# Kernel tuning notes

Hardware: AMD Instinct MI355X
Metric: run time of the kernel (lower is better)

The kernel has to match this reference:

```python
import jax, jax.numpy as jnp
import numpy as np

K = 3          # deformable conv kernel size
PAD = 1        # padding
BN_EPS = 1e-5


def _upsample2(x):
    # nn.Upsample(scale_factor=2) default mode='nearest' on [B,C,D,H,W]
    x = jnp.repeat(x, 2, axis=2)
    x = jnp.repeat(x, 2, axis=3)
    x = jnp.repeat(x, 2, axis=4)
    return x


def _conv3d(x, w, b):
    out = jax.lax.conv_general_dilated(
        x, w, window_strides=(1, 1, 1), padding=[(PAD, PAD)] * 3,
        dimension_numbers=('NCDHW', 'OIDHW', 'NCDHW'))
    return out + b[None, :, None, None, None]


def _trilinear_sample(x, coords):
    # x: [B,C,D,H,W]; coords: [B,Kt,3,D,H,W] absolute (possibly OOB) positions.
    # Zero padding outside the volume (standard deformable-conv convention).
    B, C, D, H, W = x.shape
    pd, ph, pw = coords[:, :, 0], coords[:, :, 1], coords[:, :, 2]  # [B,Kt,D,H,W]
    d0 = jnp.floor(pd); h0 = jnp.floor(ph); w0 = jnp.floor(pw)
    fd = pd - d0; fh = ph - h0; fw = pw - w0
    x_flat = x.reshape(B, C, D * H * W)

    def gather(di, hi, wi):
        valid = ((di >= 0) & (di < D) & (hi >= 0) & (hi < H) & (wi >= 0) & (wi < W))
        dc = jnp.clip(di, 0, D - 1).astype(jnp.int32)
        hc = jnp.clip(hi, 0, H - 1).astype(jnp.int32)
        wc = jnp.clip(wi, 0, W - 1).astype(jnp.int32)
        flat = (dc * H + hc) * W + wc                       # [B,Kt,D,H,W]
        vals = jax.vmap(lambda xf, idx: jnp.take(xf, idx.reshape(-1), axis=1))(x_flat, flat)
        vals = vals.reshape(B, C, *flat.shape[1:])          # [B,C,Kt,D,H,W]
        return vals * valid[:, None].astype(x.dtype)

    out = jnp.zeros((B, C) + pd.shape[1:], x.dtype)
    for dd in (0, 1):
        for hh in (0, 1):
            for ww in (0, 1):
                wgt = ((fd if dd else 1.0 - fd)
                       * (fh if hh else 1.0 - fh)
                       * (fw if ww else 1.0 - fw))           # [B,Kt,D,H,W]
                out = out + gather(d0 + dd, h0 + hh, w0 + ww) * wgt[:, None]
    return out  # [B,C,Kt,D,H,W]


def _deform_conv3d(x, w_off, b_off, w, b):
    B, C, D, H, W = x.shape
    Kt = K ** 3
    # offsets: Conv3d(C, 3*K^3, k=3, pad=1) -> [B, Kt, 3(dz,dy,dx), D,H,W]
    off = _conv3d(x, w_off, b_off).reshape(B, Kt, 3, D, H, W)
    # kernel tap displacements relative to output voxel: [Kt,3]
    taps = jnp.stack(jnp.meshgrid(jnp.arange(K), jnp.arange(K), jnp.arange(K),
                                  indexing='ij'), -1).reshape(-1, 3).astype(x.dtype) - PAD
    grid = jnp.stack(jnp.meshgrid(jnp.arange(D, dtype=x.dtype),
                                  jnp.arange(H, dtype=x.dtype),
                                  jnp.arange(W, dtype=x.dtype),
                                  indexing='ij'), 0)          # [3,D,H,W]
    coords = grid[None, None] + taps[None, :, :, None, None, None] + off  # [B,Kt,3,D,H,W]
    sampled = _trilinear_sample(x, coords)                    # [B,C,Kt,D,H,W]
    out = jnp.einsum('bckdhw,ock->bodhw', sampled, w.reshape(w.shape[0], C, Kt))
    return out + b[None, :, None, None, None]


def setup_inputs() -> dict:
    key = jax.random.key(0)
    ks = jax.random.split(key, 4)
    ch_in, ch_out = 64, 32
    x = jax.random.normal(ks[0], (1, ch_in, 16, 16, 16), jnp.float32)
    w_off = jax.random.normal(ks[1], (3 * K ** 3, ch_in, K, K, K), jnp.float32) * 0.01
    b_off = jnp.zeros((3 * K ** 3,), jnp.float32)
    w = jax.random.normal(ks[2], (ch_out, ch_in, K, K, K), jnp.float32) * 0.05
    b = jnp.zeros((ch_out,), jnp.float32)
    gamma = jnp.ones((ch_out,), jnp.float32)
    beta = jnp.zeros((ch_out,), jnp.float32)
    return {"x": x, "w_off": w_off, "b_off": b_off, "w": w, "b": b,
            "gamma": gamma, "beta": beta}


def reference(x, w_off, b_off, w, b, gamma, beta):
    x = _upsample2(x)                                  # [B,C,2D,2H,2W]
    out = _deform_conv3d(x, w_off, b_off, w, b)        # [B,ch_out,2D,2H,2W]
    # BatchNorm3d (training-mode batch stats) + ReLU
    mean = out.mean(axis=(0, 2, 3, 4), keepdims=True)
    var = out.var(axis=(0, 2, 3, 4), keepdims=True)
    out = (out - mean) * jax.lax.rsqrt(var + BN_EPS)
    out = out * gamma[None, :, None, None, None] + beta[None, :, None, None, None]
    return jax.nn.relu(out)
```

## Files before the change

kernel.cpp:

```cpp
#include <hip/hip_runtime.h>
#include <math.h>

#define NVOX  32768
#define CIN   64
#define COUT  32
#define KT    27
#define CIT   1728
#define PSP   5832

#define WS_XT   0
#define WS_WA   186624
#define WS_WO   214272
#define WS_STAT 297216
#define WS_P    297280

typedef __attribute__((ext_vector_type(8))) _Float16 half8;
typedef __attribute__((ext_vector_type(2))) _Float16 half2v;
typedef __attribute__((ext_vector_type(4))) float floatx4;

static __device__ __forceinline__ unsigned dup16(float w) {
    unsigned short b = __builtin_bit_cast(unsigned short, (_Float16)w);
    return (unsigned)b * 0x10001u;
}
static __device__ __forceinline__ half2v u2h2(unsigned u) {
    return __builtin_bit_cast(half2v, u);
}
static __device__ __forceinline__ half8 pk8(half2v a, half2v b, half2v c, half2v d) {
    union { half8 v; half2v p[4]; } u;
    u.p[0] = a; u.p[1] = b; u.p[2] = c; u.p[3] = d;
    return u.v;
}

__global__ __launch_bounds__(256) void prep_all_kernel(
        const float* __restrict__ x, const float* __restrict__ w_off,
        const float* __restrict__ wmat, float* __restrict__ ws) {
    int b = blockIdx.x, t = threadIdx.x;
    if (b < 92) {
        __shared__ _Float16 tile[64][65];
        _Float16* xth = (_Float16*)(ws + WS_XT);
        int tq = t >> 6, lane = t & 63;
        int base = b * 64;
        int cell = base + lane;
        int qw = cell % 18, qh = (cell / 18) % 18, qd = cell / 324;
        bool interior = (cell < PSP) && qd >= 1 && qd <= 16 && qh >= 1 && qh <= 16
                        && qw >= 1 && qw <= 16;
        int xbase = interior ? (((qd - 1) * 16 + (qh - 1)) * 16 + (qw - 1)) : 0;
#pragma unroll
        for (int i = 0; i < 16; i++) {
            int c = tq * 16 + i;
            float v = interior ? x[c * 4096 + xbase] : 0.f;
            tile[lane][c] = (_Float16)v;
        }
        __syncthreads();
#pragma unroll
        for (int i = 0; i < 16; i++) {
            int s = tq * 16 + i;
            int cell2 = base + s;
            if (cell2 < PSP) xth[cell2 * 64 + lane] = tile[s][lane];
        }
    } else if (b < 119) {
        _Float16* wa = (_Float16*)(ws + WS_WA);
        int idx = (b - 92) * 256 + t;
        int kb = idx >> 5, o = idx & 31;
        half8 r;
#pragma unroll
        for (int j = 0; j < 8; j++) {
            int kk = kb * 8 + j;
            int tap = kk >> 6, ci = kk & 63;
            r[j] = (_Float16)wmat[o * CIT + ci * 27 + tap];
        }
        *(half8*)(wa + idx * 8) = r;
    } else if (b < 200) {
        _Float16* wo = (_Float16*)(ws + WS_WO);
        int idx = (b - 119) * 256 + t;
        int kb = idx / 96, m = idx % 96;
        half8 r;
#pragma unroll
        for (int j = 0; j < 8; j++) {
            int kk = kb * 8 + j;
            int tap = kk >> 6, ci = kk & 63;
            float v = (m < 81) ? w_off[(m * 64 + ci) * 27 + tap] : 0.f;
            r[j] = (_Float16)v;
        }
        *(half8*)(wo + idx * 8) = r;
    } else {
        if (t < 64) ws[WS_STAT + t] = 0.f;
    }
}

__global__ __launch_bounds__(256, 4) void offset_kernel(
        const float* __restrict__ b_off, float* ws) {
    __shared__ __align__(16) _Float16 abuf[2 * 6144];
    int tid = threadIdx.x, wave = tid >> 6, lane = tid & 63;
    int nsub = wave & 1, kh = wave >> 1;
    int col = lane & 15, quad = lane >> 4;
    int pbase = blockIdx.x * 32;
    int d = blockIdx.x >> 5, h = blockIdx.x & 31;
    int vox = nsub * 16 + col;
    const char* xtb = (const char*)(ws + WS_XT);
    const int4* wsrc = (const int4*)(ws + WS_WO);
    _Float16* Pw = (_Float16*)(ws + WS_P);
    int4* ab4 = (int4*)abuf;

    int4 ra0 = wsrc[tid], ra1 = wsrc[256 + tid], ra2 = wsrc[512 + tid];
    ab4[tid] = ra0; ab4[256 + tid] = ra1; ab4[512 + tid] = ra2;
    ra0 = wsrc[768 + tid]; ra1 = wsrc[768 + 256 + tid]; ra2 = wsrc[768 + 512 + tid];
    __syncthreads();

    floatx4 acc[6];
#pragma unroll
    for (int mt = 0; mt < 6; mt++) acc[mt] = (floatx4){0.f, 0.f, 0.f, 0.f};

    int fb = (kh * 4 + quad) * 768 + col * 8;

#pragma unroll 1
    for (int tap = 0; tap < 27; tap++) {
        if (tap < 26) {
            int4* dst = ab4 + ((tap + 1) & 1) * 768;
            dst[tid] = ra0; dst[256 + tid] = ra1; dst[512 + tid] = ra2;
        }
        if (tap < 25) {
            const int4* s = wsrc + (tap + 2) * 768;
            ra0 = s[tid]; ra1 = s[256 + tid]; ra2 = s[512 + tid];
        }
        int kd = tap / 9, r9 = tap - kd * 9, kh2 = r9 / 3, kw2 = r9 - kh2 * 3;
        int rd = ((d + kd - 1) >> 1) + 1;
        int rh = ((h + kh2 - 1) >> 1) + 1;
        int rw = ((vox + kw2 - 1) >> 1) + 1;
        int cell = (rd * 18 + rh) * 18 + rw;
        int4 bx = *(const int4*)(xtb + cell * 128 + kh * 64 + quad * 16);
        half8 bfrag = __builtin_bit_cast(half8, bx);
        const _Float16* abh = abuf + (tap & 1) * 6144;
#pragma unroll
        for (int mt = 0; mt < 6; mt++) {
            half8 af = *(const half8*)(abh + fb + mt * 128);
            acc[mt] = __builtin_amdgcn_mfma_f32_16x16x32_f16(af, bfrag, acc[mt], 0, 0, 0);
        }
        __syncthreads();
    }

    float* red = (float*)abuf;
    if (kh == 1) {
#pragma unroll
        for (int mt = 0; mt < 6; mt++)
#pragma unroll
            for (int r = 0; r < 4; r++)
                red[(nsub * 96 + mt * 16 + quad * 4 + r) * 17 + col] = acc[mt][r];
    }
    __syncthreads();
    if (kh == 0) {
#pragma unroll
        for (int mt = 0; mt < 6; mt++)
#pragma unroll
            for (int r = 0; r < 4; r++) {
                int m = mt * 16 + quad * 4 + r;
                if (m < 81) {
                    float v = acc[mt][r] + red[(nsub * 96 + m) * 17 + col] + b_off[m];
                    Pw[m * NVOX + pbase + nsub * 16 + col] = (_Float16)v;
                }
            }
    }
}

#define ACCP(xl, xh, Wx) do { \
    s00 += (Wx) * u2h2((unsigned)(xl).x); s01 += (Wx) * u2h2((unsigned)(xl).y); \
    s02 += (Wx) * u2h2((unsigned)(xl).z); s03 += (Wx) * u2h2((unsigned)(xl).w); \
    s10 += (Wx) * u2h2((unsigned)(xh).x); s11 += (Wx) * u2h2((unsigned)(xh).y); \
    s12 += (Wx) * u2h2((unsigned)(xh).z); s13 += (Wx) * u2h2((unsigned)(xh).w); \
} while (0)

#define DO2(ap, wp) do { \
    int a0_ = (ap) & 0x7fff, a1_ = (int)((((unsigned)(ap)) >> 16) & 0x7fffu); \
    unsigned wl_ = ((unsigned)(wp) & 0xffffu) * 0x10001u; \
    unsigned wh_ = (((unsigned)(wp)) >> 16) * 0x10001u; \
    int4 x0l_ = *(const int4*)(region + (a0_ ^ subLo)); \
    int4 x0h_ = *(const int4*)(region + (a0_ ^ subHi)); \
    int4 x1l_ = *(const int4*)(region + (a1_ ^ subLo)); \
    int4 x1h_ = *(const int4*)(region + (a1_ ^ subHi)); \
    ACCP(x0l_, x0h_, u2h2(wl_)); ACCP(x1l_, x1h_, u2h2(wh_)); \
} while (0)

#define GSLOW(Ax, wf) do { \
    half2v Wq_ = u2h2(dup16(wf)); \
    int4 xl_ = *(const int4*)(xtb + (Ax) + subLo); \
    int4 xh_ = *(const int4*)(xtb + (Ax) + subLo + 64); \
    t00 += Wq_ * u2h2((unsigned)xl_.x); t01 += Wq_ * u2h2((unsigned)xl_.y); \
    t02 += Wq_ * u2h2((unsigned)xl_.z); t03 += Wq_ * u2h2((unsigned)xl_.w); \
    t10 += Wq_ * u2h2((unsigned)xh_.x); t11 += Wq_ * u2h2((unsigned)xh_.y); \
    t12 += Wq_ * u2h2((unsigned)xh_.z); t13 += Wq_ * u2h2((unsigned)xh_.w); \
} while (0)

__global__ __launch_bounds__(256, 4) void deform_kernel(
        const float* __restrict__ bias, float* ws, float* __restrict__ out) {
    __shared__ __align__(16) char region[25600];
    __shared__ __align__(16) int2 scratch[4][16][4];
    __shared__ float pbuf[2][2][16][17];
    __shared__ float rsum[COUT], rsq[COUT];

    int tid = threadIdx.x, wave = tid >> 6, lane = tid & 63;
    int col = lane & 15, quad = lane >> 4;
    int bid = blockIdx.x;
    int d0 = (bid >> 6) << 1, h0 = ((bid >> 2) & 15) << 1, w0 = (bid & 3) << 3;

    const char* xtb = (const char*)(ws + WS_XT);
    const half8* wa8 = (const half8*)(ws + WS_WA);
    const _Float16* P = (const _Float16*)(ws + WS_P);
    float* gstat = ws + WS_STAT;

    if (tid < COUT) { rsum[tid] = 0.f; rsq[tid] = 0.f; }

    int pdlo = (d0 >> 1) - 1, phlo = (h0 >> 1) - 1, pwlo = (w0 >> 1) - 1;

#pragma unroll 1
    for (int it = 0; it < 7; it++) {
        int i = it * 256 + tid;
        if (i < 1600) {
            int r = i >> 3, c16 = i & 7;
            int rd = r / 40, rem = r - rd * 40, rh = rem >> 3, rw = rem & 7;
            int pd = min(max(pdlo + rd, 0), 17);
            int ph = min(max(phlo + rh, 0), 17);
            int pw = min(max(pwlo + rw, 0), 17);
            int cell = (pd * 18 + ph) * 18 + pw;
            int4 vsrc = *(const int4*)(xtb + cell * 128 + c16 * 16);
            *(int4*)(region + r * 128 + ((c16 * 16) ^ ((r & 7) << 4))) = vsrc;
        }
    }
    __syncthreads();

    int vh = wave & 1, kt = wave >> 1;
    int v = vh * 16 + col;
    int dv = v >> 4, hv = (v >> 3) & 1, wv = v & 7;
    int dcoord = d0 + dv, hcoord = h0 + hv, wcoord = w0 + wv;
    int gvox = dcoord * 1024 + hcoord * 32 + wcoord;
    int tbeg = kt ? 14 : 0, tend = kt ? 27 : 14;
    int subLo = quad * 16, subHi = subLo + 64;
    int bd = quad >> 1, bh = quad & 1;

    floatx4 acc0 = {0.f, 0.f, 0.f, 0.f}, acc1 = {0.f, 0.f, 0.f, 0.f};

    float od = (float)P[(3 * tbeg + 0) * NVOX + gvox];
    float oh = (float)P[(3 * tbeg + 1) * NVOX + gvox];
    float ow = (float)P[(3 * tbeg + 2) * NVOX + gvox];

#pragma unroll 1
    for (int tap = tbeg; tap < tend; tap++) {
        int kd = tap / 9, r9 = tap - kd * 9, kh2 = r9 / 3, kw2 = r9 - kh2 * 3;
        float pdc = (float)(dcoord + kd - 1) + od;
        float phc = (float)(hcoord + kh2 - 1) + oh;
        float pwc = (float)(wcoord + kw2 - 1) + ow;
        float fd0 = floorf(pdc), fh0 = floorf(phc), fw0 = floorf(pwc);
        float fd = pdc - fd0, fh = phc - fh0, fw = pwc - fw0;
        int id = (int)fd0, ih = (int)fh0, iw = (int)fw0;

        int cd0 = ((min(max(id,     -2), 33)) >> 1) + 1;
        int cd1 = ((min(max(id + 1, -2), 33)) >> 1) + 1;
        int ch0 = ((min(max(ih,     -2), 33)) >> 1) + 1;
        int ch1 = ((min(max(ih + 1, -2), 33)) >> 1) + 1;
        int cw0 = ((min(max(iw,     -2), 33)) >> 1) + 1;
        int cw1 = ((min(max(iw + 1, -2), 33)) >> 1) + 1;
        int sd0 = cd0 - pdlo, sd1 = cd1 - pdlo;
        int sh0 = ch0 - phlo, sh1 = ch1 - phlo;
        int sw0 = cw0 - pwlo, sw1 = cw1 - pwlo;
        bool oob = ((unsigned)sd0 > 4u) | ((unsigned)sd1 > 4u)
                 | ((unsigned)sh0 > 4u) | ((unsigned)sh1 > 4u)
                 | ((unsigned)sw0 > 7u) | ((unsigned)sw1 > 7u);

        int sdq = bd ? sd1 : sd0, shq = bh ? sh1 : sh0;
        int rb = (sdq * 5 + shq) * 8;
        int r0 = rb + sw0, r1 = rb + sw1;
        int a0 = oob ? 0x8000 : ((r0 << 7) | ((r0 & 7) << 4));
        int a1 = oob ? 0x8000 : ((r1 << 7) | ((r1 & 7) << 4));
        float gdw = 1.f - fd, ghw = 1.f - fh, gww = 1.f - fw;
        float wd = bd ? fd : gdw, wh = bh ? fh : ghw;
        float wdh = wd * wh;
        unsigned wb0 = (unsigned)__builtin_bit_cast(unsigned short, (_Float16)(wdh * gww));
        unsigned wb1 = (unsigned)__builtin_bit_cast(unsigned short, (_Float16)(wdh * fw));
        scratch[wave][col][quad] = make_int2(a0 | (a1 << 16), (int)(wb0 | (wb1 << 16)));

        if (tap + 1 < tend) {
            od = (float)P[(3 * tap + 3) * NVOX + gvox];
            oh = (float)P[(3 * tap + 4) * NVOX + gvox];
            ow = (float)P[(3 * tap + 5) * NVOX + gvox];
        }

        int kb = tap * 8 + quad;
        half8 a00 = wa8[kb * 32 + col];
        half8 a01 = wa8[kb * 32 + 16 + col];
        half8 a10 = wa8[(kb + 4) * 32 + col];
        half8 a11 = wa8[(kb + 4) * 32 + 16 + col];

        const int4* sc = (const int4*)&scratch[wave][col][0];
        int4 p0 = sc[0], p1 = sc[1];

        half2v s00 = {0, 0}, s01 = {0, 0}, s02 = {0, 0}, s03 = {0, 0};
        half2v s10 = {0, 0}, s11 = {0, 0}, s12 = {0, 0}, s13 = {0, 0};
        DO2(p0.x, p0.y); DO2(p0.z, p0.w);
        DO2(p1.x, p1.y); DO2(p1.z, p1.w);

        if (__any((p0.x & 0x8000) != 0)) {
            bool flg = (p0.x & 0x8000) != 0;
            int Rd0 = ((min(max(id,     -2), 33) >> 1) + 1) * (324 * 128);
            int Rd1 = ((min(max(id + 1, -2), 33) >> 1) + 1) * (324 * 128);
            int Rh0 = ((min(max(ih,     -2), 33) >> 1) + 1) * (18 * 128);
            int Rh1 = ((min(max(ih + 1, -2), 33) >> 1) + 1) * (18 * 128);
            int Rw0 = ((min(max(iw,     -2), 33) >> 1) + 1) * 128;
            int Rw1 = ((min(max(iw + 1, -2), 33) >> 1) + 1) * 128;
            half2v t00 = {0,0}, t01 = {0,0}, t02 = {0,0}, t03 = {0,0};
            half2v t10 = {0,0}, t11 = {0,0}, t12 = {0,0}, t13 = {0,0};
            GSLOW(Rd0 + Rh0 + Rw0, gdw * ghw * gww);
            GSLOW(Rd0 + Rh0 + Rw1, gdw * ghw * fw);
            GSLOW(Rd0 + Rh1 + Rw0, gdw * fh  * gww);
            GSLOW(Rd0 + Rh1 + Rw1, gdw * fh  * fw);
            GSLOW(Rd1 + Rh0 + Rw0, fd  * ghw * gww);
            GSLOW(Rd1 + Rh0 + Rw1, fd  * ghw * fw);
            GSLOW(Rd1 + Rh1 + Rw0, fd  * fh  * gww);
            GSLOW(Rd1 + Rh1 + Rw1, fd  * fh  * fw);
            s00 = flg ? t00 : s00; s01 = flg ? t01 : s01;
            s02 = flg ? t02 : s02; s03 = flg ? t03 : s03;
            s10 = flg ? t10 : s10; s11 = flg ? t11 : s11;
            s12 = flg ? t12 : s12; s13 = flg ? t13 : s13;
        }

        half8 bf0 = pk8(s00, s01, s02, s03);
        half8 bf1 = pk8(s10, s11, s12, s13);

        acc0 = __builtin_amdgcn_mfma_f32_16x16x32_f16(a00, bf0, acc0, 0, 0, 0);
        acc1 = __builtin_amdgcn_mfma_f32_16x16x32_f16(a01, bf0, acc1, 0, 0, 0);
        acc0 = __builtin_amdgcn_mfma_f32_16x16x32_f16(a10, bf1, acc0, 0, 0, 0);
        acc1 = __builtin_amdgcn_mfma_f32_16x16x32_f16(a11, bf1, acc1, 0, 0, 0);
    }

    __syncthreads();
    if (kt == 1) {
#pragma unroll
        for (int r = 0; r < 4; r++) {
            pbuf[vh][0][quad * 4 + r][col] = acc0[r];
            pbuf[vh][1][quad * 4 + r][col] = acc1[r];
        }
    }
    __syncthreads();
    if (kt == 0) {
#pragma unroll
        for (int r = 0; r < 4; r++) {
            int i = quad * 4 + r;
            int o0 = i;
            float v0 = acc0[r] + pbuf[vh][0][i][col] + bias[o0];
            out[o0 * NVOX + gvox] = v0;
            atomicAdd(&rsum[o0], v0);
            atomicAdd(&rsq[o0], v0 * v0);
            int o1 = 16 + i;
            float v1 = acc1[r] + pbuf[vh][1][i][col] + bias[o1];
            out[o1 * NVOX + gvox] = v1;
            atomicAdd(&rsum[o1], v1);
            atomicAdd(&rsq[o1], v1 * v1);
        }
    }
    __syncthreads();
    if (tid < COUT) {
        atomicAdd(&gstat[tid], rsum[tid]);
        atomicAdd(&gstat[COUT + tid], rsq[tid]);
    }
}

__global__ void bn_kernel(const float* __restrict__ ws,
                          const float* __restrict__ gamma,
                          const float* __restrict__ beta,
                          float* out) {
    int i = blockIdx.x * 256 + threadIdx.x;
    int o = i >> 15;
    const float* gstat = ws + WS_STAT;
    const float inv = 1.f / 32768.f;
    float mean = gstat[o] * inv;
    float var  = gstat[COUT + o] * inv - mean * mean;
    float sc   = rsqrtf(var + 1e-5f) * gamma[o];
    float v = (out[i] - mean) * sc + beta[o];
    out[i] = fmaxf(v, 0.f);
}

extern "C" void kernel_launch(void* const* d_in, const int* in_sizes, int n_in,
                              void* d_out, int out_size, void* d_ws, size_t ws_size,
                              hipStream_t stream) {
    const float* x     = (const float*)d_in[0];
    const float* w_off = (const float*)d_in[1];
    const float* b_off = (const float*)d_in[2];
    const float* wmat  = (const float*)d_in[3];
    const float* bias  = (const float*)d_in[4];
    const float* gamma = (const float*)d_in[5];
    const float* beta  = (const float*)d_in[6];
    float* ws  = (float*)d_ws;
    float* out = (float*)d_out;

    prep_all_kernel<<<201, 256, 0, stream>>>(x, w_off, wmat, ws);
    offset_kernel<<<1024, 256, 0, stream>>>(b_off, ws);
    deform_kernel<<<1024, 256, 0, stream>>>(bias, ws, out);
    bn_kernel<<<4096, 256, 0, stream>>>(ws, gamma, beta, out);
}
```

Measured before the change: 146.3 us.

## Fold nearest-upsample into offset conv weights as 8 parity-phase 2x2x2 convs

The offset conv on the nearest-upsampled input is rewritten as eight parity-specific 2x2x2 convolutions on the low-res input. Each phase gets its own pre-summed fp16 weight set, built in the prep kernel. This cuts the offset GEMM's K dimension from 27 taps to 8 and lets B fragments be loaded up front. Separately, deform_kernel reuses the region buffer for its reduction scratch, raises its occupancy hint to 5, and changes the LDS swizzle. The costs are a larger workspace, more prep work, and strided writes to the P buffer.

```diff
diff --git a/kernel.cpp b/kernel.cpp
--- a/kernel.cpp
+++ b/kernel.cpp
@@ -10,9 +10,9 @@
 
 #define WS_XT   0
 #define WS_WA   186624
-#define WS_WO   214272
-#define WS_STAT 297216
-#define WS_P    297280
+#define WS_W2   214272
+#define WS_STAT 410880
+#define WS_P    410944
 
 typedef __attribute__((ext_vector_type(8))) _Float16 half8;
 typedef __attribute__((ext_vector_type(2))) _Float16 half2v;
@@ -70,19 +70,36 @@
             r[j] = (_Float16)wmat[o * CIT + ci * 27 + tap];
         }
         *(half8*)(wa + idx * 8) = r;
-    } else if (b < 200) {
-        _Float16* wo = (_Float16*)(ws + WS_WO);
+    } else if (b < 311) {
+        _Float16* w2 = (_Float16*)(ws + WS_W2);
         int idx = (b - 119) * 256 + t;
-        int kb = idx / 96, m = idx % 96;
+        int pi = idx / 6144;
+        int rem = idx - pi * 6144;
+        int kb = rem / 96, m = rem - (rem / 96) * 96;
+        int pid = pi >> 2, pih = (pi >> 1) & 1, piw = pi & 1;
         half8 r;
 #pragma unroll
         for (int j = 0; j < 8; j++) {
             int kk = kb * 8 + j;
-            int tap = kk >> 6, ci = kk & 63;
-            float v = (m < 81) ? w_off[(m * 64 + ci) * 27 + tap] : 0.f;
-            r[j] = (_Float16)v;
-        }
-        *(half8*)(wo + idx * 8) = r;
+            int tap2 = kk >> 6, ci = kk & 63;
+            int cd = tap2 >> 2, ch = (tap2 >> 1) & 1, cw = tap2 & 1;
+            int bd = pid ? (cd ? 2 : 0) : cd;
+            int nd = pid ? (cd ? 1 : 2) : (cd ? 2 : 1);
+            int bh = pih ? (ch ? 2 : 0) : ch;
+            int nh = pih ? (ch ? 1 : 2) : (ch ? 2 : 1);
+            int bw = piw ? (cw ? 2 : 0) : cw;
+            int nw = piw ? (cw ? 1 : 2) : (cw ? 2 : 1);
+            float s = 0.f;
+            if (m < 81) {
+                const float* wp = w_off + (m * 64 + ci) * 27;
+                for (int a = 0; a < nd; a++)
+                    for (int bb = 0; bb < nh; bb++)
+                        for (int c = 0; c < nw; c++)
+                            s += wp[(bd + a) * 9 + (bh + bb) * 3 + (bw + c)];
+            }
+            r[j] = (_Float16)s;
+        }
+        *(half8*)(w2 + idx * 8) = r;
     } else {
         if (t < 64) ws[WS_STAT + t] = 0.f;
     }
@@ -94,13 +111,22 @@
     int tid = threadIdx.x, wave = tid >> 6, lane = tid & 63;
     int nsub = wave & 1, kh = wave >> 1;
     int col = lane & 15, quad = lane >> 4;
-    int pbase = blockIdx.x * 32;
-    int d = blockIdx.x >> 5, h = blockIdx.x & 31;
-    int vox = nsub * 16 + col;
+    int bid = blockIdx.x;
+    int pi = bid >> 7, tile = bid & 127;
+    int pid = pi >> 2, pih = (pi >> 1) & 1, piw = pi & 1;
+    int qd = tile >> 3, qh = (tile & 7) * 2 + nsub;
     const char* xtb = (const char*)(ws + WS_XT);
-    const int4* wsrc = (const int4*)(ws + WS_WO);
+    const int4* wsrc = (const int4*)(ws + WS_W2) + pi * 6144;
     _Float16* Pw = (_Float16*)(ws + WS_P);
     int4* ab4 = (int4*)abuf;
+
+    int4 bx[8];
+#pragma unroll
+    for (int tap = 0; tap < 8; tap++) {
+        int cd = tap >> 2, ch = (tap >> 1) & 1, cw = tap & 1;
+        int cell = ((qd + cd + pid) * 18 + (qh + ch + pih)) * 18 + (col + cw + piw);
+        bx[tap] = *(const int4*)(xtb + cell * 128 + kh * 64 + quad * 16);
+    }
 
     int4 ra0 = wsrc[tid], ra1 = wsrc[256 + tid], ra2 = wsrc[512 + tid];
     ab4[tid] = ra0; ab4[256 + tid] = ra1; ab4[512 + tid] = ra2;
@@ -113,23 +139,17 @@
 
     int fb = (kh * 4 + quad) * 768 + col * 8;
 
-#pragma unroll 1
-    for (int tap = 0; tap < 27; tap++) {
-        if (tap < 26) {
+#pragma unroll
+    for (int tap = 0; tap < 8; tap++) {
+        if (tap < 7) {
             int4* dst = ab4 + ((tap + 1) & 1) * 768;
             dst[tid] = ra0; dst[256 + tid] = ra1; dst[512 + tid] = ra2;
         }
-        if (tap < 25) {
-            const int4* s = wsrc + (tap + 2) * 768;
-            ra0 = s[tid]; ra1 = s[256 + tid]; ra2 = s[512 + tid];
-        }
-        int kd = tap / 9, r9 = tap - kd * 9, kh2 = r9 / 3, kw2 = r9 - kh2 * 3;
-        int rd = ((d + kd - 1) >> 1) + 1;
-        int rh = ((h + kh2 - 1) >> 1) + 1;
-        int rw = ((vox + kw2 - 1) >> 1) + 1;
-        int cell = (rd * 18 + rh) * 18 + rw;
-        int4 bx = *(const int4*)(xtb + cell * 128 + kh * 64 + quad * 16);
-        half8 bfrag = __builtin_bit_cast(half8, bx);
+        if (tap < 6) {
+            const int4* s2 = wsrc + (tap + 2) * 768;
+            ra0 = s2[tid]; ra1 = s2[256 + tid]; ra2 = s2[512 + tid];
+        }
+        half8 bfrag = __builtin_bit_cast(half8, bx[tap]);
         const _Float16* abh = abuf + (tap & 1) * 6144;
 #pragma unroll
         for (int mt = 0; mt < 6; mt++) {
@@ -149,6 +169,8 @@
     }
     __syncthreads();
     if (kh == 0) {
+        int d = 2 * qd + pid, h = 2 * qh + pih;
+        int vbase = (d * 32 + h) * 32 + piw;
 #pragma unroll
         for (int mt = 0; mt < 6; mt++)
 #pragma unroll
@@ -156,7 +178,7 @@
                 int m = mt * 16 + quad * 4 + r;
                 if (m < 81) {
                     float v = acc[mt][r] + red[(nsub * 96 + m) * 17 + col] + b_off[m];
-                    Pw[m * NVOX + pbase + nsub * 16 + col] = (_Float16)v;
+                    Pw[m * NVOX + vbase + 2 * col] = (_Float16)v;
                 }
             }
     }
@@ -190,12 +212,13 @@
     t12 += Wq_ * u2h2((unsigned)xh_.z); t13 += Wq_ * u2h2((unsigned)xh_.w); \
 } while (0)
 
-__global__ __launch_bounds__(256, 4) void deform_kernel(
+__global__ __launch_bounds__(256, 5) void deform_kernel(
         const float* __restrict__ bias, float* ws, float* __restrict__ out) {
     __shared__ __align__(16) char region[25600];
-    __shared__ __align__(16) int2 scratch[4][16][4];
-    __shared__ float pbuf[2][2][16][17];
-    __shared__ float rsum[COUT], rsq[COUT];
+    __shared__ __align__(16) int2 scratch[4][16][6];
+    float* pbuf = (float*)region;
+    float* rsumS = (float*)(region + 8704);
+    float* rsqS  = (float*)(region + 8704 + 128);
 
     int tid = threadIdx.x, wave = tid >> 6, lane = tid & 63;
     int col = lane & 15, quad = lane >> 4;
@@ -206,8 +229,6 @@
     const half8* wa8 = (const half8*)(ws + WS_WA);
     const _Float16* P = (const _Float16*)(ws + WS_P);
     float* gstat = ws + WS_STAT;
-
-    if (tid < COUT) { rsum[tid] = 0.f; rsq[tid] = 0.f; }
 
     int pdlo = (d0 >> 1) - 1, phlo = (h0 >> 1) - 1, pwlo = (w0 >> 1) - 1;
 
@@ -222,7 +243,8 @@
             int pw = min(max(pwlo + rw, 0), 17);
             int cell = (pd * 18 + ph) * 18 + pw;
             int4 vsrc = *(const int4*)(xtb + cell * 128 + c16 * 16);
-            *(int4*)(region + r * 128 + ((c16 * 16) ^ ((r & 7) << 4))) = vsrc;
+            int f = (r ^ (r >> 3)) & 7;
+            *(int4*)(region + r * 128 + ((c16 ^ f) << 4)) = vsrc;
         }
     }
     __syncthreads();
@@ -268,8 +290,9 @@
         int sdq = bd ? sd1 : sd0, shq = bh ? sh1 : sh0;
         int rb = (sdq * 5 + shq) * 8;
         int r0 = rb + sw0, r1 = rb + sw1;
-        int a0 = oob ? 0x8000 : ((r0 << 7) | ((r0 & 7) << 4));
-        int a1 = oob ? 0x8000 : ((r1 << 7) | ((r1 & 7) << 4));
+        int f0 = (r0 ^ (r0 >> 3)) & 7, f1 = (r1 ^ (r1 >> 3)) & 7;
+        int a0 = oob ? 0x8000 : ((r0 << 7) | (f0 << 4));
+        int a1 = oob ? 0x8000 : ((r1 << 7) | (f1 << 4));
         float gdw = 1.f - fd, ghw = 1.f - fh, gww = 1.f - fw;
         float wd = bd ? fd : gdw, wh = bh ? fh : ghw;
         float wdh = wd * wh;
@@ -334,31 +357,32 @@
     if (kt == 1) {
 #pragma unroll
         for (int r = 0; r < 4; r++) {
-            pbuf[vh][0][quad * 4 + r][col] = acc0[r];
-            pbuf[vh][1][quad * 4 + r][col] = acc1[r];
-        }
-    }
+            pbuf[((vh * 2 + 0) * 16 + quad * 4 + r) * 17 + col] = acc0[r];
+            pbuf[((vh * 2 + 1) * 16 + quad * 4 + r) * 17 + col] = acc1[r];
+        }
+    }
+    if (tid < 64) ((float*)(region + 8704))[tid] = 0.f;
     __syncthreads();
     if (kt == 0) {
 #pragma unroll
         for (int r = 0; r < 4; r++) {
             int i = quad * 4 + r;
             int o0 = i;
-            float v0 = acc0[r] + pbuf[vh][0][i][col] + bias[o0];
+            float v0 = acc0[r] + pbuf[((vh * 2 + 0) * 16 + i) * 17 + col] + bias[o0];
             out[o0 * NVOX + gvox] = v0;
-            atomicAdd(&rsum[o0], v0);
-            atomicAdd(&rsq[o0], v0 * v0);
+            atomicAdd(&rsumS[o0], v0);
+            atomicAdd(&rsqS[o0], v0 * v0);
             int o1 = 16 + i;
-            float v1 = acc1[r] + pbuf[vh][1][i][col] + bias[o1];
+            float v1 = acc1[r] + pbuf[((vh * 2 + 1) * 16 + i) * 17 + col] + bias[o1];
             out[o1 * NVOX + gvox] = v1;
-            atomicAdd(&rsum[o1], v1);
-            atomicAdd(&rsq[o1], v1 * v1);
+            atomicAdd(&rsumS[o1], v1);
+            atomicAdd(&rsqS[o1], v1 * v1);
         }
     }
     __syncthreads();
     if (tid < COUT) {
-        atomicAdd(&gstat[tid], rsum[tid]);
-        atomicAdd(&gstat[COUT + tid], rsq[tid]);
+        atomicAdd(&gstat[tid], rsumS[tid]);
+        atomicAdd(&gstat[COUT + tid], rsqS[tid]);
     }
 }
 
@@ -390,7 +414,7 @@
     float* ws  = (float*)d_ws;
     float* out = (float*)d_out;
 
-    prep_all_kernel<<<201, 256, 0, stream>>>(x, w_off, wmat, ws);
+    prep_all_kernel<<<312, 256, 0, stream>>>(x, w_off, wmat, ws);
     offset_kernel<<<1024, 256, 0, stream>>>(b_off, ws);
     deform_kernel<<<1024, 256, 0, stream>>>(bias, ws, out);
     bn_kernel<<<4096, 256, 0, stream>>>(ws, gamma, beta, out);
```

Result: faster. 140.4 us (-4.1%).

## Fuse offset conv into deformable conv kernel with offsets kept in LDS

Applied to the files above, without the earlier changes.

Removes the separate offset_kernel and computes the 81 offset channels per block inside the deform kernel. The results go to an LDS tile instead of a global fp16 buffer, which cuts one launch and the global round-trip of the offset tensor. The offset MFMA loop is reorganized to split M across waves instead of K, with prefetch of the next tap's input fragment. It also changes the LDS swizzle for the gathered region and pads the scratch layout to reduce bank conflicts. In exchange, shared memory per block grows, which may lower occupancy.

```diff
diff --git a/kernel.cpp b/kernel.cpp
--- a/kernel.cpp
+++ b/kernel.cpp
@@ -12,7 +12,6 @@
 #define WS_WA   186624
 #define WS_WO   214272
 #define WS_STAT 297216
-#define WS_P    297280
 
 typedef __attribute__((ext_vector_type(8))) _Float16 half8;
 typedef __attribute__((ext_vector_type(2))) _Float16 half2v;
@@ -88,80 +87,6 @@
     }
 }
 
-__global__ __launch_bounds__(256, 4) void offset_kernel(
-        const float* __restrict__ b_off, float* ws) {
-    __shared__ __align__(16) _Float16 abuf[2 * 6144];
-    int tid = threadIdx.x, wave = tid >> 6, lane = tid & 63;
-    int nsub = wave & 1, kh = wave >> 1;
-    int col = lane & 15, quad = lane >> 4;
-    int pbase = blockIdx.x * 32;
-    int d = blockIdx.x >> 5, h = blockIdx.x & 31;
-    int vox = nsub * 16 + col;
-    const char* xtb = (const char*)(ws + WS_XT);
-    const int4* wsrc = (const int4*)(ws + WS_WO);
-    _Float16* Pw = (_Float16*)(ws + WS_P);
-    int4* ab4 = (int4*)abuf;
-
-    int4 ra0 = wsrc[tid], ra1 = wsrc[256 + tid], ra2 = wsrc[512 + tid];
-    ab4[tid] = ra0; ab4[256 + tid] = ra1; ab4[512 + tid] = ra2;
-    ra0 = wsrc[768 + tid]; ra1 = wsrc[768 + 256 + tid]; ra2 = wsrc[768 + 512 + tid];
-    __syncthreads();
-
-    floatx4 acc[6];
-#pragma unroll
-    for (int mt = 0; mt < 6; mt++) acc[mt] = (floatx4){0.f, 0.f, 0.f, 0.f};
-
-    int fb = (kh * 4 + quad) * 768 + col * 8;
-
-#pragma unroll 1
-    for (int tap = 0; tap < 27; tap++) {
-        if (tap < 26) {
-            int4* dst = ab4 + ((tap + 1) & 1) * 768;
-            dst[tid] = ra0; dst[256 + tid] = ra1; dst[512 + tid] = ra2;
-        }
-        if (tap < 25) {
-            const int4* s = wsrc + (tap + 2) * 768;
-            ra0 = s[tid]; ra1 = s[256 + tid]; ra2 = s[512 + tid];
-        }
-        int kd = tap / 9, r9 = tap - kd * 9, kh2 = r9 / 3, kw2 = r9 - kh2 * 3;
-        int rd = ((d + kd - 1) >> 1) + 1;
-        int rh = ((h + kh2 - 1) >> 1) + 1;
-        int rw = ((vox + kw2 - 1) >> 1) + 1;
-        int cell = (rd * 18 + rh) * 18 + rw;
-        int4 bx = *(const int4*)(xtb + cell * 128 + kh * 64 + quad * 16);
-        half8 bfrag = __builtin_bit_cast(half8, bx);
-        const _Float16* abh = abuf + (tap & 1) * 6144;
-#pragma unroll
-        for (int mt = 0; mt < 6; mt++) {
-            half8 af = *(const half8*)(abh + fb + mt * 128);
-            acc[mt] = __builtin_amdgcn_mfma_f32_16x16x32_f16(af, bfrag, acc[mt], 0, 0, 0);
-        }
-        __syncthreads();
-    }
-
-    float* red = (float*)abuf;
-    if (kh == 1) {
-#pragma unroll
-        for (int mt = 0; mt < 6; mt++)
-#pragma unroll
-            for (int r = 0; r < 4; r++)
-                red[(nsub * 96 + mt * 16 + quad * 4 + r) * 17 + col] = acc[mt][r];
-    }
-    __syncthreads();
-    if (kh == 0) {
-#pragma unroll
-        for (int mt = 0; mt < 6; mt++)
-#pragma unroll
-            for (int r = 0; r < 4; r++) {
-                int m = mt * 16 + quad * 4 + r;
-                if (m < 81) {
-                    float v = acc[mt][r] + red[(nsub * 96 + m) * 17 + col] + b_off[m];
-                    Pw[m * NVOX + pbase + nsub * 16 + col] = (_Float16)v;
-                }
-            }
-    }
-}
-
 #define ACCP(xl, xh, Wx) do { \
     s00 += (Wx) * u2h2((unsigned)(xl).x); s01 += (Wx) * u2h2((unsigned)(xl).y); \
     s02 += (Wx) * u2h2((unsigned)(xl).z); s03 += (Wx) * u2h2((unsigned)(xl).w); \
@@ -190,12 +115,16 @@
     t12 += Wq_ * u2h2((unsigned)xh_.z); t13 += Wq_ * u2h2((unsigned)xh_.w); \
 } while (0)
 
-__global__ __launch_bounds__(256, 4) void deform_kernel(
-        const float* __restrict__ bias, float* ws, float* __restrict__ out) {
-    __shared__ __align__(16) char region[25600];
-    __shared__ __align__(16) int2 scratch[4][16][4];
-    __shared__ float pbuf[2][2][16][17];
-    __shared__ float rsum[COUT], rsq[COUT];
+__global__ __launch_bounds__(256, 4) void fused_kernel(
+        const float* __restrict__ b_off, const float* __restrict__ bias,
+        float* ws, float* __restrict__ out) {
+    __shared__ __align__(16) char shmem[34816];
+    char* region = shmem;
+    int2* scratch2 = (int2*)(shmem + 25600);
+    _Float16* Pl = (_Float16*)(shmem + 28672);
+    float* pbuf = (float*)shmem;
+    float* rsumS = (float*)(shmem + 8704);
+    float* rsqS  = (float*)(shmem + 8832);
 
     int tid = threadIdx.x, wave = tid >> 6, lane = tid & 63;
     int col = lane & 15, quad = lane >> 4;
@@ -204,10 +133,81 @@
 
     const char* xtb = (const char*)(ws + WS_XT);
     const half8* wa8 = (const half8*)(ws + WS_WA);
-    const _Float16* P = (const _Float16*)(ws + WS_P);
     float* gstat = ws + WS_STAT;
 
-    if (tid < COUT) { rsum[tid] = 0.f; rsq[tid] = 0.f; }
+    {
+        int4* ab4 = (int4*)shmem;
+        const _Float16* abuf16 = (const _Float16*)shmem;
+        const int4* wsrc = (const int4*)(ws + WS_WO);
+        int nsub = wave & 1, mh = wave >> 1;
+        int vv = nsub * 16 + col;
+        int dA = d0 + (vv >> 4), hA = h0 + ((vv >> 3) & 1), wA = w0 + (vv & 7);
+
+        int4 ra0 = wsrc[tid], ra1 = wsrc[256 + tid], ra2 = wsrc[512 + tid];
+        ab4[tid] = ra0; ab4[256 + tid] = ra1; ab4[512 + tid] = ra2;
+        ra0 = wsrc[768 + tid]; ra1 = wsrc[768 + 256 + tid]; ra2 = wsrc[768 + 512 + tid];
+
+        int c0;
+        {
+            int rd = ((dA - 1) >> 1) + 1, rh = ((hA - 1) >> 1) + 1, rw = ((wA - 1) >> 1) + 1;
+            c0 = (rd * 18 + rh) * 18 + rw;
+        }
+        int4 bx0 = *(const int4*)(xtb + c0 * 128 + quad * 16);
+        int4 bx1 = *(const int4*)(xtb + c0 * 128 + 64 + quad * 16);
+        __syncthreads();
+
+        floatx4 oacc[3];
+#pragma unroll
+        for (int mt = 0; mt < 3; mt++) oacc[mt] = (floatx4){0.f, 0.f, 0.f, 0.f};
+
+#pragma unroll 1
+        for (int tap = 0; tap < 27; tap++) {
+            if (tap < 26) {
+                int4* dst = ab4 + ((tap + 1) & 1) * 768;
+                dst[tid] = ra0; dst[256 + tid] = ra1; dst[512 + tid] = ra2;
+            }
+            if (tap < 25) {
+                const int4* s2 = wsrc + (tap + 2) * 768;
+                ra0 = s2[tid]; ra1 = s2[256 + tid]; ra2 = s2[512 + tid];
+            }
+            int4 nbx0 = bx0, nbx1 = bx1;
+            if (tap < 26) {
+                int tn = tap + 1;
+                int kd = tn / 9, r9 = tn - kd * 9, kh2 = r9 / 3, kw2 = r9 - kh2 * 3;
+                int rd = ((dA + kd - 1) >> 1) + 1;
+                int rh = ((hA + kh2 - 1) >> 1) + 1;
+                int rw = ((wA + kw2 - 1) >> 1) + 1;
+                int nc = (rd * 18 + rh) * 18 + rw;
+                nbx0 = *(const int4*)(xtb + nc * 128 + quad * 16);
+                nbx1 = *(const int4*)(xtb + nc * 128 + 64 + quad * 16);
+            }
+            const _Float16* abh = abuf16 + (tap & 1) * 6144;
+            half8 bf0 = __builtin_bit_cast(half8, bx0);
+            half8 bf1 = __builtin_bit_cast(half8, bx1);
+#pragma unroll
+            for (int mt = 0; mt < 3; mt++) {
+                half8 a0 = *(const half8*)(abh + quad * 768 + (mh * 48 + mt * 16 + col) * 8);
+                oacc[mt] = __builtin_amdgcn_mfma_f32_16x16x32_f16(a0, bf0, oacc[mt], 0, 0, 0);
+            }
+#pragma unroll
+            for (int mt = 0; mt < 3; mt++) {
+                half8 a1 = *(const half8*)(abh + (4 + quad) * 768 + (mh * 48 + mt * 16 + col) * 8);
+                oacc[mt] = __builtin_amdgcn_mfma_f32_16x16x32_f16(a1, bf1, oacc[mt], 0, 0, 0);
+            }
+            bx0 = nbx0; bx1 = nbx1;
+            __syncthreads();
+        }
+
+#pragma unroll
+        for (int mt = 0; mt < 3; mt++)
+#pragma unroll
+            for (int r = 0; r < 4; r++) {
+                int m = mh * 48 + mt * 16 + quad * 4 + r;
+                if (m < 81)
+                    Pl[m * 32 + vv] = (_Float16)(oacc[mt][r] + b_off[m]);
+            }
+        __syncthreads();
+    }
 
     int pdlo = (d0 >> 1) - 1, phlo = (h0 >> 1) - 1, pwlo = (w0 >> 1) - 1;
 
@@ -222,7 +222,8 @@
             int pw = min(max(pwlo + rw, 0), 17);
             int cell = (pd * 18 + ph) * 18 + pw;
             int4 vsrc = *(const int4*)(xtb + cell * 128 + c16 * 16);
-            *(int4*)(region + r * 128 + ((c16 * 16) ^ ((r & 7) << 4))) = vsrc;
+            int f = (r ^ (r >> 3)) & 7;
+            *(int4*)(region + r * 128 + ((c16 ^ f) << 4)) = vsrc;
         }
     }
     __syncthreads();
@@ -238,9 +239,9 @@
 
     floatx4 acc0 = {0.f, 0.f, 0.f, 0.f}, acc1 = {0.f, 0.f, 0.f, 0.f};
 
-    float od = (float)P[(3 * tbeg + 0) * NVOX + gvox];
-    float oh = (float)P[(3 * tbeg + 1) * NVOX + gvox];
-    float ow = (float)P[(3 * tbeg + 2) * NVOX + gvox];
+    float od = (float)Pl[(3 * tbeg + 0) * 32 + v];
+    float oh = (float)Pl[(3 * tbeg + 1) * 32 + v];
+    float ow = (float)Pl[(3 * tbeg + 2) * 32 + v];
 
 #pragma unroll 1
     for (int tap = tbeg; tap < tend; tap++) {
@@ -268,19 +269,21 @@
         int sdq = bd ? sd1 : sd0, shq = bh ? sh1 : sh0;
         int rb = (sdq * 5 + shq) * 8;
         int r0 = rb + sw0, r1 = rb + sw1;
-        int a0 = oob ? 0x8000 : ((r0 << 7) | ((r0 & 7) << 4));
-        int a1 = oob ? 0x8000 : ((r1 << 7) | ((r1 & 7) << 4));
+        int f0 = (r0 ^ (r0 >> 3)) & 7, f1 = (r1 ^ (r1 >> 3)) & 7;
+        int a0 = oob ? 0x8000 : ((r0 << 7) | (f0 << 4));
+        int a1 = oob ? 0x8000 : ((r1 << 7) | (f1 << 4));
         float gdw = 1.f - fd, ghw = 1.f - fh, gww = 1.f - fw;
         float wd = bd ? fd : gdw, wh = bh ? fh : ghw;
         float wdh = wd * wh;
         unsigned wb0 = (unsigned)__builtin_bit_cast(unsigned short, (_Float16)(wdh * gww));
         unsigned wb1 = (unsigned)__builtin_bit_cast(unsigned short, (_Float16)(wdh * fw));
-        scratch[wave][col][quad] = make_int2(a0 | (a1 << 16), (int)(wb0 | (wb1 << 16)));
+        scratch2[(wave * 16 + col) * 6 + quad] =
+            make_int2(a0 | (a1 << 16), (int)(wb0 | (wb1 << 16)));
 
         if (tap + 1 < tend) {
-            od = (float)P[(3 * tap + 3) * NVOX + gvox];
-            oh = (float)P[(3 * tap + 4) * NVOX + gvox];
-            ow = (float)P[(3 * tap + 5) * NVOX + gvox];
+            od = (float)Pl[(3 * tap + 3) * 32 + v];
+            oh = (float)Pl[(3 * tap + 4) * 32 + v];
+            ow = (float)Pl[(3 * tap + 5) * 32 + v];
         }
 
         int kb = tap * 8 + quad;
@@ -289,7 +292,7 @@
         half8 a10 = wa8[(kb + 4) * 32 + col];
         half8 a11 = wa8[(kb + 4) * 32 + 16 + col];
 
-        const int4* sc = (const int4*)&scratch[wave][col][0];
+        const int4* sc = (const int4*)(scratch2 + (wave * 16 + col) * 6);
         int4 p0 = sc[0], p1 = sc[1];
 
         half2v s00 = {0, 0}, s01 = {0, 0}, s02 = {0, 0}, s03 = {0, 0};
@@ -334,31 +337,32 @@
     if (kt == 1) {
 #pragma unroll
         for (int r = 0; r < 4; r++) {
-            pbuf[vh][0][quad * 4 + r][col] = acc0[r];
-            pbuf[vh][1][quad * 4 + r][col] = acc1[r];
-        }
-    }
+            pbuf[((vh * 2 + 0) * 16 + quad * 4 + r) * 17 + col] = acc0[r];
+            pbuf[((vh * 2 + 1) * 16 + quad * 4 + r) * 17 + col] = acc1[r];
+        }
+    }
+    if (tid < 64) ((float*)(shmem + 8704))[tid] = 0.f;
     __syncthreads();
     if (kt == 0) {
 #pragma unroll
         for (int r = 0; r < 4; r++) {
             int i = quad * 4 + r;
             int o0 = i;
-            float v0 = acc0[r] + pbuf[vh][0][i][col] + bias[o0];
+            float v0 = acc0[r] + pbuf[((vh * 2 + 0) * 16 + i) * 17 + col] + bias[o0];
             out[o0 * NVOX + gvox] = v0;
-            atomicAdd(&rsum[o0], v0);
-            atomicAdd(&rsq[o0], v0 * v0);
+            atomicAdd(&rsumS[o0], v0);
+            atomicAdd(&rsqS[o0], v0 * v0);
             int o1 = 16 + i;
-            float v1 = acc1[r] + pbuf[vh][1][i][col] + bias[o1];
+            float v1 = acc1[r] + pbuf[((vh * 2 + 1) * 16 + i) * 17 + col] + bias[o1];
             out[o1 * NVOX + gvox] = v1;
-            atomicAdd(&rsum[o1], v1);
-            atomicAdd(&rsq[o1], v1 * v1);
+            atomicAdd(&rsumS[o1], v1);
+            atomicAdd(&rsqS[o1], v1 * v1);
         }
     }
     __syncthreads();
     if (tid < COUT) {
-        atomicAdd(&gstat[tid], rsum[tid]);
-        atomicAdd(&gstat[COUT + tid], rsq[tid]);
+        atomicAdd(&gstat[tid], rsumS[tid]);
+        atomicAdd(&gstat[COUT + tid], rsqS[tid]);
     }
 }
 
@@ -391,7 +395,6 @@
     float* out = (float*)d_out;
 
     prep_all_kernel<<<201, 256, 0, stream>>>(x, w_off, wmat, ws);
-    offset_kernel<<<1024, 256, 0, stream>>>(b_off, ws);
-    deform_kernel<<<1024, 256, 0, stream>>>(bias, ws, out);
+    fused_kernel<<<1024, 256, 0, stream>>>(b_off, bias, ws, out);
     bn_kernel<<<4096, 256, 0, stream>>>(ws, gamma, beta, out);
 }
```

Result: no change. 145.1 us (-0.8%).
